# Kernel optimization log

Measured on AMD Instinct MI355X. Metric: run time of the kernel, lower is better.

## Reference

```python
import jax, jax.numpy as jnp
import numpy as np

T, H = 4096, 2048

def _glorot(key, shape):
    return jax.random.uniform(key, shape, minval=-1.0, maxval=1.0) * jnp.sqrt(2.0 / sum(shape))

def setup_inputs() -> dict:
    key = jax.random.key(0)
    k_x, k_a, k_b = jax.random.split(key, 3)
    x_seq = jax.random.normal(k_x, (T, H), dtype=jnp.float32)
    a_diag = _glorot(k_a, (H,)).astype(jnp.float32)        # (H,)
    b_mat = _glorot(k_b, (H, H)).astype(jnp.float32)       # (H, H)
    return {"x_seq": x_seq, "a_diag": a_diag, "b_mat": b_mat}

def _power_kernel(a_diag, length):
    # kernel[h, k] = a_diag[h] ** k for k in [0, length).
    # Computed via cumprod (identical math to jnp.power with integer exponents,
    # but well-defined for negative a_diag and differentiable).
    h = a_diag.shape[0]
    ones = jnp.ones((h, 1), dtype=a_diag.dtype)
    pows = jnp.cumprod(jnp.broadcast_to(a_diag[:, None], (h, length - 1)), axis=1)
    return jnp.concatenate([ones, pows], axis=1)[:, None, :]  # (H, 1, T)

def reference(x_seq, a_diag, b_mat):
    seq_len, hidden_size = x_seq.shape
    s = b_mat.T @ x_seq.T                                  # (H, T)
    s_padded = jnp.pad(s, ((0, 0), (seq_len - 1, 0)))[None, :, :]  # (1, H, 2T-1)
    kernel = _power_kernel(a_diag, seq_len)                # (H, 1, T)
    kernel_flipped = jnp.flip(kernel, axis=-1)
    conv_out = jax.lax.conv_general_dilated(
        s_padded, kernel_flipped,
        window_strides=(1,), padding="VALID",
        dimension_numbers=("NCT", "OIT", "NCT"),
        feature_group_count=hidden_size,
    )                                                      # (1, H, T)
    return conv_out[0].T                                   # (T, H)
```

## Files before the change

### kernel.cpp

```cpp
#include <hip/hip_runtime.h>
#include <cstdint>
#include <cstddef>

typedef short bf16x8 __attribute__((ext_vector_type(8)));
typedef float f32x4 __attribute__((ext_vector_type(4)));

__device__ __forceinline__ unsigned short f2bf(float f) {
    union { float f; uint32_t u; } v; v.f = f;
    uint32_t r = v.u + 0x7FFFu + ((v.u >> 16) & 1u);
    return (unsigned short)(r >> 16);
}

__device__ __forceinline__ float bf2f(unsigned short u) {
    union { uint32_t u; float f; } v; v.u = (uint32_t)u << 16;
    return v.f;
}


__global__ void prep_kernel(const float* __restrict__ X,
                            unsigned short* __restrict__ Xbf, int n4,
                            const float* __restrict__ B,
                            unsigned short* __restrict__ Bt, int H,
                            int castBlocks) {
    if ((int)blockIdx.x < castBlocks) {
        int i = blockIdx.x * 256 + threadIdx.x;
        if (i < n4) {
            float4 v = ((const float4*)X)[i];
            ushort4 o;
            o.x = f2bf(v.x); o.y = f2bf(v.y); o.z = f2bf(v.z); o.w = f2bf(v.w);
            ((ushort4*)Xbf)[i] = o;
        }
        return;
    }
    __shared__ float tile[32][33];
    int tb = blockIdx.x - castBlocks;
    int tilesPerRow = H / 32;
    int bx = (tb % tilesPerRow) * 32;
    int by = (tb / tilesPerRow) * 32;
    int tx = threadIdx.x & 31, ty = threadIdx.x >> 5;
#pragma unroll
    for (int i = 0; i < 32; i += 8)
        tile[ty + i][tx] = B[(size_t)(by + ty + i) * H + bx + tx];
    __syncthreads();
#pragma unroll
    for (int i = 0; i < 32; i += 8)
        Bt[(size_t)(bx + ty + i) * H + by + tx] = f2bf(tile[tx][ty + i]);
}


__global__ __launch_bounds__(256, 2) void gemm_sk_bf16out(
    const unsigned short* __restrict__ A,
    const unsigned short* __restrict__ Bt,
    unsigned short* __restrict__ S0, unsigned short* __restrict__ S1,
    int M, int N, int K, int gridM, int gridN)
{
    __shared__ __attribute__((aligned(16))) unsigned short sA[256 * 64];
    __shared__ __attribute__((aligned(16))) unsigned short sB[128 * 64];

    const int tid  = threadIdx.x;
    const int wave = tid >> 6;
    const int lane = tid & 63;

    int b = blockIdx.x;
    int mt, nt, kt;
    if ((gridM & 7) == 0) {
        int x = b & 7, g = b >> 3;
        int mPerX = gridM >> 3;
        int ml = g % mPerX, g2 = g / mPerX;
        nt = g2 % gridN;
        kt = g2 / gridN;
        mt = x * mPerX + ml;
    } else {
        mt = b % gridM;
        nt = (b / gridM) % gridN;
        kt = b / (gridM * gridN);
    }
    const int m0 = mt * 256;
    const int n0 = nt * 128;
    const int ksize = K / 2;
    const int kbase = kt * ksize;

    const int srow = lane >> 3;
    const int scol = ((lane & 7) ^ srow) * 8;

    const int quad = lane >> 4;
    const int l16  = lane & 15;
    const int wm = wave >> 1;
    const int wn = wave & 1;
    const int s7 = l16 & 7;
    const int c0 = (quad ^ s7) * 16;
    const int c1 = ((quad + 4) ^ s7) * 16;

    f32x4 acc[8][4];
#pragma unroll
    for (int i = 0; i < 8; ++i)
#pragma unroll
        for (int j = 0; j < 4; ++j)
            acc[i][j] = (f32x4){0.f, 0.f, 0.f, 0.f};

    const unsigned short* Ab = A  + (size_t)m0 * K;
    const unsigned short* Bb = Bt + (size_t)n0 * K;

    const int rA = (wm * 16 + (l16 >> 3)) * 1024 + s7 * 128;
    const int rB = (wn * 8  + (l16 >> 3)) * 1024 + s7 * 128;

    for (int k0 = kbase; k0 < kbase + ksize; k0 += 64) {
#pragma unroll
        for (int i = 0; i < 8; ++i) {
            const int t = wave * 8 + i;
            const unsigned short* ga = Ab + (size_t)(t * 8 + srow) * K + (k0 + scol);
            __builtin_amdgcn_global_load_lds(
                (const __attribute__((address_space(1))) void*)ga,
                (__attribute__((address_space(3))) void*)(sA + t * 512),
                16, 0, 0);
        }
#pragma unroll
        for (int i = 0; i < 4; ++i) {
            const int t = wave * 4 + i;
            const unsigned short* gb = Bb + (size_t)(t * 8 + srow) * K + (k0 + scol);
            __builtin_amdgcn_global_load_lds(
                (const __attribute__((address_space(1))) void*)gb,
                (__attribute__((address_space(3))) void*)(sB + t * 512),
                16, 0, 0);
        }
        __syncthreads();

#pragma unroll
        for (int kk = 0; kk < 2; ++kk) {
            const int co = kk ? c1 : c0;
            bf16x8 af[8], bfr[4];
#pragma unroll
            for (int im = 0; im < 8; ++im)
                af[im] = *(const bf16x8*)((const char*)sA + rA + im * 2048 + co);
#pragma unroll
            for (int in = 0; in < 4; ++in)
                bfr[in] = *(const bf16x8*)((const char*)sB + rB + in * 2048 + co);
#pragma unroll
            for (int im = 0; im < 8; ++im)
#pragma unroll
                for (int in = 0; in < 4; ++in)
                    acc[im][in] = __builtin_amdgcn_mfma_f32_16x16x32_bf16(
                        af[im], bfr[in], acc[im][in], 0, 0, 0);
        }
        __syncthreads();
    }

    unsigned short* __restrict__ S = (kt == 0) ? S0 : S1;
#pragma unroll
    for (int im = 0; im < 8; ++im) {
#pragma unroll
        for (int in = 0; in < 4; ++in) {
            int col = n0 + wn * 64 + in * 16 + l16;
#pragma unroll
            for (int r = 0; r < 4; ++r) {
                int row = m0 + wm * 128 + im * 16 + quad * 4 + r;
                S[(size_t)row * N + col] = f2bf(acc[im][in][r]);
            }
        }
    }
}


__device__ __forceinline__ void stage_tile128(
    const unsigned short* __restrict__ Ab, const unsigned short* __restrict__ Bb,
    unsigned short* sAp, unsigned short* sBp,
    int wave, int srow, int scol, int k0, int K)
{
#pragma unroll
    for (int i = 0; i < 4; ++i) {
        const int t = wave * 4 + i;
        const unsigned short* ga = Ab + (size_t)(t * 8 + srow) * K + (k0 + scol);
        __builtin_amdgcn_global_load_lds(
            (const __attribute__((address_space(1))) void*)ga,
            (__attribute__((address_space(3))) void*)(sAp + t * 512),
            16, 0, 0);
        const unsigned short* gb = Bb + (size_t)(t * 8 + srow) * K + (k0 + scol);
        __builtin_amdgcn_global_load_lds(
            (const __attribute__((address_space(1))) void*)gb,
            (__attribute__((address_space(3))) void*)(sBp + t * 512),
            16, 0, 0);
    }
}

__global__ __launch_bounds__(256, 4) void gemm_f32out(
    const unsigned short* __restrict__ A,
    const unsigned short* __restrict__ Bt,
    float* __restrict__ C, int M, int N, int K, int gridM)
{
    __shared__ __attribute__((aligned(16))) unsigned short sA[128 * 64];
    __shared__ __attribute__((aligned(16))) unsigned short sB[128 * 64];

    const int tid  = threadIdx.x;
    const int wave = tid >> 6;
    const int lane = tid & 63;

    int b = blockIdx.x;
    int mt, nt;
    if ((gridM & 7) == 0) {
        int x = b & 7, g = b >> 3;
        int mPerX = gridM >> 3;
        mt = x * mPerX + (g % mPerX);
        nt = g / mPerX;
    } else {
        mt = b % gridM;
        nt = b / gridM;
    }
    const int m0 = mt * 128;
    const int n0 = nt * 128;

    const int srow = lane >> 3;
    const int scol = ((lane & 7) ^ srow) * 8;
    const int quad = lane >> 4;
    const int l16  = lane & 15;
    const int wm = wave >> 1;
    const int wn = wave & 1;
    const int s7 = l16 & 7;
    const int rbaseA = (wm * 8 + (l16 >> 3)) * 1024 + s7 * 128;
    const int rbaseB = (wn * 8 + (l16 >> 3)) * 1024 + s7 * 128;
    const int coff0 = (quad ^ s7) * 16;
    const int coff1 = ((quad + 4) ^ s7) * 16;

    f32x4 acc[4][4];
#pragma unroll
    for (int i = 0; i < 4; ++i)
#pragma unroll
        for (int j = 0; j < 4; ++j)
            acc[i][j] = (f32x4){0.f, 0.f, 0.f, 0.f};

    const unsigned short* Ab = A  + (size_t)m0 * K;
    const unsigned short* Bb = Bt + (size_t)n0 * K;

    for (int k0 = 0; k0 < K; k0 += 64) {
        stage_tile128(Ab, Bb, sA, sB, wave, srow, scol, k0, K);
        __syncthreads();
        bf16x8 af[2][4], bfr[2][4];
#pragma unroll
        for (int t = 0; t < 4; ++t) {
            const char* pa = (const char*)sA + rbaseA + t * 2048;
            af[0][t]  = *(const bf16x8*)(pa + coff0);
            af[1][t]  = *(const bf16x8*)(pa + coff1);
            const char* pb = (const char*)sB + rbaseB + t * 2048;
            bfr[0][t] = *(const bf16x8*)(pb + coff0);
            bfr[1][t] = *(const bf16x8*)(pb + coff1);
        }
#pragma unroll
        for (int kk = 0; kk < 2; ++kk)
#pragma unroll
            for (int im = 0; im < 4; ++im)
#pragma unroll
                for (int in = 0; in < 4; ++in)
                    acc[im][in] = __builtin_amdgcn_mfma_f32_16x16x32_bf16(
                        af[kk][im], bfr[kk][in], acc[im][in], 0, 0, 0);
        __syncthreads();
    }

#pragma unroll
    for (int im = 0; im < 4; ++im)
#pragma unroll
        for (int in = 0; in < 4; ++in) {
            int col = n0 + wn * 64 + in * 16 + l16;
#pragma unroll
            for (int r = 0; r < 4; ++r) {
                int row = m0 + wm * 64 + im * 16 + quad * 4 + r;
                C[(size_t)row * N + col] = acc[im][in][r];
            }
        }
}


__global__ void scan_splitk_bf16(const unsigned short* __restrict__ S0,
                                 const unsigned short* __restrict__ S1,
                                 const float* __restrict__ a_diag,
                                 float* __restrict__ out,
                                 int H2, int chunk) {
    int tid = blockIdx.x * blockDim.x + threadIdx.x;
    int hp = tid % H2, c = tid / H2;
    float2 av = ((const float2*)a_diag)[hp];
    const ushort2* S0v = (const ushort2*)S0;
    const ushort2* S1v = (const ushort2*)S1;
    float2* outv = (float2*)out;

    float y0 = 0.f, y1 = 0.f;
    if (c > 0) {
        size_t r0 = (size_t)c * chunk - 8;
#pragma unroll
        for (int i = 0; i < 8; ++i) {
            size_t idx = (r0 + i) * H2 + hp;
            ushort2 u = S0v[idx], w = S1v[idx];
            y0 = fmaf(av.x, y0, bf2f(u.x) + bf2f(w.x));
            y1 = fmaf(av.y, y1, bf2f(u.y) + bf2f(w.y));
        }
    }
    size_t idx = (size_t)c * chunk * H2 + hp;
    ushort2 u = S0v[idx], w = S1v[idx];
    for (int t = 0; t < chunk - 1; ++t) {
        size_t idx2 = idx + H2;
        ushort2 un = S0v[idx2], wn = S1v[idx2];
        y0 = fmaf(av.x, y0, bf2f(u.x) + bf2f(w.x));
        y1 = fmaf(av.y, y1, bf2f(u.y) + bf2f(w.y));
        outv[idx] = make_float2(y0, y1);
        u = un; w = wn; idx = idx2;
    }
    y0 = fmaf(av.x, y0, bf2f(u.x) + bf2f(w.x));
    y1 = fmaf(av.y, y1, bf2f(u.y) + bf2f(w.y));
    outv[idx] = make_float2(y0, y1);
}


__global__ void scan_init_kernel(const float* __restrict__ S,
                                 const float* __restrict__ a_diag,
                                 float* __restrict__ yinit,
                                 int H, int chunk, int W) {
    int tid = blockIdx.x * blockDim.x + threadIdx.x;
    int h = tid % H, c = tid / H;
    float a = a_diag[h];
    float y = 0.f;
    if (c > 0) {
        int t0 = c * chunk;
        for (int t = t0 - W; t < t0; ++t)
            y = fmaf(a, y, S[(size_t)t * H + h]);
    }
    yinit[(size_t)c * H + h] = y;
}

__global__ void scan_run_kernel(const float* __restrict__ yinit,
                                const float* __restrict__ a_diag,
                                float* __restrict__ out,
                                int H, int chunk) {
    int tid = blockIdx.x * blockDim.x + threadIdx.x;
    int h = tid % H, c = tid / H;
    float a = a_diag[h];
    float y = yinit[(size_t)c * H + h];
    size_t base = (size_t)c * chunk * H + h;
    float s = out[base];
#pragma unroll 4
    for (int t = 0; t < chunk - 1; ++t) {
        float snext = out[base + (size_t)(t + 1) * H];
        y = fmaf(a, y, s);
        out[base + (size_t)t * H] = y;
        s = snext;
    }
    y = fmaf(a, y, s);
    out[base + (size_t)(chunk - 1) * H] = y;
}


__global__ void gemm_fallback(const float* __restrict__ X, const float* __restrict__ B,
                              float* __restrict__ C, int M, int N, int K) {
    __shared__ float sA[16][17];
    __shared__ float sB[16][17];
    int tx = threadIdx.x, ty = threadIdx.y;
    int row = blockIdx.y * 16 + ty, col = blockIdx.x * 16 + tx;
    float acc = 0.f;
    for (int k0 = 0; k0 < K; k0 += 16) {
        sA[ty][tx] = (row < M && k0 + tx < K) ? X[(size_t)row * K + k0 + tx] : 0.f;
        sB[ty][tx] = (k0 + ty < K && col < N) ? B[(size_t)(k0 + ty) * N + col] : 0.f;
        __syncthreads();
#pragma unroll
        for (int kk = 0; kk < 16; ++kk) acc += sA[ty][kk] * sB[kk][tx];
        __syncthreads();
    }
    if (row < M && col < N) C[(size_t)row * N + col] = acc;
}

__global__ void scan_serial(float* __restrict__ out, const float* __restrict__ a_diag,
                            int T, int H) {
    int h = blockIdx.x * blockDim.x + threadIdx.x;
    if (h >= H) return;
    float a = a_diag[h], y = 0.f;
    for (int t = 0; t < T; ++t) {
        y = fmaf(a, y, out[(size_t)t * H + h]);
        out[(size_t)t * H + h] = y;
    }
}


extern "C" void kernel_launch(void* const* d_in, const int* in_sizes, int n_in,
                              void* d_out, int out_size, void* d_ws, size_t ws_size,
                              hipStream_t stream) {
    const float* x = (const float*)d_in[0];
    const float* a = (const float*)d_in[1];
    const float* b = (const float*)d_in[2];
    float* out = (float*)d_out;

    const int H = in_sizes[1];
    const int T = in_sizes[0] / H;
    const int M = T, N = H, K = H;

    const int CHUNK = 16, W = 12;

    size_t xbf_elems = (size_t)M * K;
    size_t bt_elems  = (size_t)N * K;
    size_t MN = (size_t)M * N;
    int nchunks = (T % CHUNK == 0) ? T / CHUNK : 0;

    size_t need_sk  = (xbf_elems + bt_elems + 2 * MN) * 2 + 256;
    size_t need_mid = xbf_elems * 2 + bt_elems * 2 + 256;

    bool shape_ok = (M % 128 == 0) && (N % 128 == 0) && (K % 128 == 0) &&
                    (H % 32 == 0) && nchunks > 0 && ((xbf_elems % 4) == 0) &&
                    (((size_t)nchunks * H) % 256 == 0);
    int gridMf = M / 128;
    int gridM  = (M % 256 == 0) ? M / 256 : 0;
    int gridN  = N / 128;

    int n4 = (int)(xbf_elems / 4);
    int castBlocks = (n4 + 255) / 256;
    int transBlocks = (H % 32 == 0) ? (H / 32) * (H / 32) : 0;

    int H2 = H / 2;
    size_t nth2 = (size_t)nchunks * H2;

    if (shape_ok && gridM > 0 && (gridM % 8 == 0) && (H % 4 == 0) &&
        (nth2 % 256 == 0) && ws_size >= need_sk) {
        unsigned short* Xbf = (unsigned short*)d_ws;
        unsigned short* Bt  = Xbf + xbf_elems;
        unsigned short* S0  = Bt + bt_elems;
        unsigned short* S1  = S0 + MN;

        prep_kernel<<<castBlocks + transBlocks, 256, 0, stream>>>(
            x, Xbf, n4, b, Bt, H, castBlocks);

        gemm_sk_bf16out<<<gridM * gridN * 2, 256, 0, stream>>>(
            Xbf, Bt, S0, S1, M, N, K, gridM, gridN);

        scan_splitk_bf16<<<(int)(nth2 / 256), 256, 0, stream>>>(
            S0, S1, a, out, H2, CHUNK);
    } else if (shape_ok && ws_size >= need_mid &&
               ((size_t)nchunks * H * 4 <= xbf_elems * 2)) {
        unsigned short* Xbf = (unsigned short*)d_ws;
        unsigned short* Bt  = Xbf + xbf_elems;
        float* yinit = (float*)d_ws;

        prep_kernel<<<castBlocks + transBlocks, 256, 0, stream>>>(
            x, Xbf, n4, b, Bt, H, castBlocks);

        gemm_f32out<<<gridMf * gridN, 256, 0, stream>>>(
            Xbf, Bt, out, M, N, K, gridMf);

        int nth = nchunks * H;
        scan_init_kernel<<<nth / 256, 256, 0, stream>>>(out, a, yinit, H, CHUNK, W);
        scan_run_kernel<<<nth / 256, 256, 0, stream>>>(yinit, a, out, H, CHUNK);
    } else {
        dim3 tb(16, 16), tg((N + 15) / 16, (M + 15) / 16);
        gemm_fallback<<<tg, tb, 0, stream>>>(x, b, out, M, N, K);
        scan_serial<<<(H + 255) / 256, 256, 0, stream>>>(out, a, T, H);
    }
}
```

Baseline: 139.8 us.

## Add 256x256 eight-phase pipelined split-K GEMM with direct global-to-LDS loads

Adds a new bf16 GEMM kernel that uses 512 threads and 256x256 output tiles. It stages operands with global_load_lds into 128KB of dynamic LDS using double buffering and an XOR swizzle, and interleaves LDS reads, async global loads and MFMA bursts across eight barrier-separated phases with setprio. The aim is to raise arithmetic intensity and hide global-memory latency better than the previous 256x128 split-K kernel. In exchange it needs high LDS and register use, which limits occupancy, and it issues many barriers.

```diff
diff --git a/kernel.cpp b/kernel.cpp
--- a/kernel.cpp
+++ b/kernel.cpp
@@ -45,6 +45,202 @@
 #pragma unroll
     for (int i = 0; i < 32; i += 8)
         Bt[(size_t)(bx + ty + i) * H + by + tx] = f2bf(tile[tx][ty + i]);
+}
+
+
+#define G8_FENCE __builtin_amdgcn_sched_barrier(0)
+#define G8_BAR   __builtin_amdgcn_s_barrier()
+#define G8_LGKM0 asm volatile("s_waitcnt lgkmcnt(0)" ::: "memory")
+#define G8_VM4   asm volatile("s_waitcnt vmcnt(4)" ::: "memory")
+#define G8_VM0   asm volatile("s_waitcnt vmcnt(0)" ::: "memory")
+
+#define G8_STAGE(gbase, lbase, h, k0) do {                                    \
+    const int c0_ = (h) * 16 + wave;                                          \
+    const int c1_ = c0_ + 8;                                                  \
+    __builtin_amdgcn_global_load_lds(                                         \
+        (const __attribute__((address_space(1))) void*)                       \
+            ((gbase) + (size_t)(c0_ * 8 + srow) * K + ((k0) + scol)),         \
+        (__attribute__((address_space(3))) void*)                             \
+            ((lbase) + c0_ * 1024 + lane * 16), 16, 0, 0);                    \
+    __builtin_amdgcn_global_load_lds(                                         \
+        (const __attribute__((address_space(1))) void*)                       \
+            ((gbase) + (size_t)(c1_ * 8 + srow) * K + ((k0) + scol)),         \
+        (__attribute__((address_space(3))) void*)                             \
+            ((lbase) + c1_ * 1024 + lane * 16), 16, 0, 0);                    \
+} while (0)
+
+#define G8_LOAD_AF(buf, imh) do {                                             \
+    const char* p_ = (const char*)(buf) + rA + (imh) * 8192;                  \
+    af[0][0] = *(const bf16x8*)(p_ + 0 * 2048 + koff0);                       \
+    af[0][1] = *(const bf16x8*)(p_ + 0 * 2048 + koff1);                       \
+    af[1][0] = *(const bf16x8*)(p_ + 1 * 2048 + koff0);                       \
+    af[1][1] = *(const bf16x8*)(p_ + 1 * 2048 + koff1);                       \
+    af[2][0] = *(const bf16x8*)(p_ + 2 * 2048 + koff0);                       \
+    af[2][1] = *(const bf16x8*)(p_ + 2 * 2048 + koff1);                       \
+    af[3][0] = *(const bf16x8*)(p_ + 3 * 2048 + koff0);                       \
+    af[3][1] = *(const bf16x8*)(p_ + 3 * 2048 + koff1);                       \
+} while (0)
+
+#define G8_LOAD_BF(buf, inh) do {                                             \
+    const char* p_ = (const char*)(buf) + rB + (inh) * 4096;                  \
+    bq[inh][0][0] = *(const bf16x8*)(p_ + 0 * 2048 + koff0);                  \
+    bq[inh][0][1] = *(const bf16x8*)(p_ + 0 * 2048 + koff1);                  \
+    bq[inh][1][0] = *(const bf16x8*)(p_ + 1 * 2048 + koff0);                  \
+    bq[inh][1][1] = *(const bf16x8*)(p_ + 1 * 2048 + koff1);                  \
+} while (0)
+
+#define G8_MFMA(imh, inh) do {                                                \
+    _Pragma("unroll")                                                         \
+    for (int j_ = 0; j_ < 4; ++j_) {                                          \
+        acc[(imh)*4+j_][(inh)*2+0] = __builtin_amdgcn_mfma_f32_16x16x32_bf16( \
+            af[j_][0], bq[inh][0][0], acc[(imh)*4+j_][(inh)*2+0], 0, 0, 0);   \
+        acc[(imh)*4+j_][(inh)*2+0] = __builtin_amdgcn_mfma_f32_16x16x32_bf16( \
+            af[j_][1], bq[inh][0][1], acc[(imh)*4+j_][(inh)*2+0], 0, 0, 0);   \
+        acc[(imh)*4+j_][(inh)*2+1] = __builtin_amdgcn_mfma_f32_16x16x32_bf16( \
+            af[j_][0], bq[inh][1][0], acc[(imh)*4+j_][(inh)*2+1], 0, 0, 0);   \
+        acc[(imh)*4+j_][(inh)*2+1] = __builtin_amdgcn_mfma_f32_16x16x32_bf16( \
+            af[j_][1], bq[inh][1][1], acc[(imh)*4+j_][(inh)*2+1], 0, 0, 0);   \
+    }                                                                         \
+} while (0)
+
+#define G8_TAIL(MF, VMW) do {                                                 \
+    G8_FENCE;                                                                 \
+    G8_BAR;                                                                   \
+    G8_LGKM0; G8_FENCE;                                                       \
+    __builtin_amdgcn_s_setprio(1);                                            \
+    MF;                                                                       \
+    __builtin_amdgcn_s_setprio(0);                                            \
+    G8_FENCE; VMW;                                                            \
+    G8_BAR;                                                                   \
+    asm volatile("" ::: "memory");                                            \
+    G8_FENCE;                                                                 \
+} while (0)
+
+__global__ __launch_bounds__(512, 2) void gemm_8ph_bf16out(
+    const unsigned short* __restrict__ A,
+    const unsigned short* __restrict__ Bt,
+    unsigned short* __restrict__ S0, unsigned short* __restrict__ S1,
+    int M, int N, int K, int gridM2, int gridN2)
+{
+    extern __shared__ char smem[];
+
+    const int tid  = threadIdx.x;
+    const int wave = tid >> 6;
+    const int lane = tid & 63;
+
+    int b = blockIdx.x;
+    int mt, nt, kt;
+    if ((gridM2 & 7) == 0) {
+        int x = b & 7, g = b >> 3;
+        int mPerX = gridM2 >> 3;
+        int ml = g % mPerX, g2 = g / mPerX;
+        nt = g2 % gridN2;
+        kt = g2 / gridN2;
+        mt = x * mPerX + ml;
+    } else {
+        mt = b % gridM2;
+        nt = (b / gridM2) % gridN2;
+        kt = b / (gridM2 * gridN2);
+    }
+    const int m0 = mt * 256;
+    const int n0 = nt * 256;
+    const int ksize = K >> 1;
+    const int kbase = kt * ksize;
+    const int NT = ksize >> 6;
+    const int NI = NT >> 1;
+
+    const int wm = wave >> 2;
+    const int wn = wave & 3;
+    const int srow = lane >> 3;
+    const int scol = ((lane & 7) ^ srow) * 8;
+    const int quad = lane >> 4;
+    const int l16  = lane & 15;
+    const int s7   = l16 & 7;
+    const int rA = (wm * 16 + (l16 >> 3)) * 1024 + s7 * 128;
+    const int rB = (wn * 8  + (l16 >> 3)) * 1024 + s7 * 128;
+    const int koff0 = (quad ^ s7) * 16;
+    const int koff1 = ((quad + 4) ^ s7) * 16;
+
+    char* const A0L = smem;
+    char* const A1L = smem + 32768;
+    char* const B0L = smem + 65536;
+    char* const B1L = smem + 98304;
+
+    const unsigned short* const Ag = A  + (size_t)m0 * K;
+    const unsigned short* const Bg = Bt + (size_t)n0 * K;
+
+    f32x4 acc[8][4];
+#pragma unroll
+    for (int i = 0; i < 8; ++i)
+#pragma unroll
+        for (int j = 0; j < 4; ++j)
+            acc[i][j] = (f32x4){0.f, 0.f, 0.f, 0.f};
+    bf16x8 af[4][2];
+    bf16x8 bq[2][2][2];
+
+    G8_STAGE(Bg, B0L, 0, kbase);
+    G8_STAGE(Bg, B0L, 1, kbase);
+    G8_STAGE(Ag, A0L, 0, kbase);
+    G8_STAGE(Ag, A0L, 1, kbase);
+    G8_STAGE(Bg, B1L, 0, kbase + 64);
+    G8_STAGE(Bg, B1L, 1, kbase + 64);
+    G8_FENCE; G8_VM4;
+    G8_BAR;
+    asm volatile("" ::: "memory");
+    G8_FENCE;
+
+#pragma unroll 1
+    for (int it = 0; it < NI; ++it) {
+        const int c0t = it * 2;
+        int t1 = c0t + 1; if (t1 > NT - 1) t1 = NT - 1;
+        int t2 = c0t + 2; if (t2 > NT - 1) t2 = NT - 1;
+        int t3 = c0t + 3; if (t3 > NT - 1) t3 = NT - 1;
+        const int k1 = kbase + t1 * 64;
+        const int k2 = kbase + t2 * 64;
+        const int k3 = kbase + t3 * 64;
+
+        G8_LOAD_AF(A0L, 0);
+        G8_LOAD_BF(B0L, 0);
+        G8_STAGE(Ag, A1L, 0, k1);
+        G8_TAIL(G8_MFMA(0, 0), (void)0);
+        G8_LOAD_BF(B0L, 1);
+        G8_STAGE(Ag, A1L, 1, k1);
+        G8_TAIL(G8_MFMA(0, 1), (void)0);
+        G8_LOAD_AF(A0L, 1);
+        G8_STAGE(Bg, B0L, 0, k2);
+        G8_TAIL(G8_MFMA(1, 1), (void)0);
+        G8_STAGE(Bg, B0L, 1, k2);
+        G8_TAIL(G8_MFMA(1, 0), G8_VM4);
+
+        G8_LOAD_AF(A1L, 0);
+        G8_LOAD_BF(B1L, 0);
+        G8_STAGE(Ag, A0L, 0, k2);
+        G8_TAIL(G8_MFMA(0, 0), (void)0);
+        G8_LOAD_BF(B1L, 1);
+        G8_STAGE(Ag, A0L, 1, k2);
+        G8_TAIL(G8_MFMA(0, 1), (void)0);
+        G8_LOAD_AF(A1L, 1);
+        G8_STAGE(Bg, B1L, 0, k3);
+        G8_TAIL(G8_MFMA(1, 1), (void)0);
+        G8_STAGE(Bg, B1L, 1, k3);
+        G8_TAIL(G8_MFMA(1, 0), G8_VM4);
+    }
+
+    G8_VM0;
+
+    unsigned short* __restrict__ S = (kt == 0) ? S0 : S1;
+#pragma unroll
+    for (int im = 0; im < 8; ++im) {
+#pragma unroll
+        for (int in = 0; in < 4; ++in) {
+            const int col = n0 + wn * 64 + in * 16 + l16;
+#pragma unroll
+            for (int r = 0; r < 4; ++r) {
+                const int row = m0 + wm * 128 + im * 16 + quad * 4 + r;
+                S[(size_t)row * N + col] = f2bf(acc[im][in][r]);
+            }
+        }
+    }
 }
 
 
@@ -403,6 +599,9 @@
     int gridMf = M / 128;
     int gridM  = (M % 256 == 0) ? M / 256 : 0;
     int gridN  = N / 128;
+    int gridM8 = (M % 256 == 0) ? M / 256 : 0;
+    int gridN8 = (N % 256 == 0) ? N / 256 : 0;
+    bool k8ok  = (K % 256 == 0) && (K >= 256);
 
     int n4 = (int)(xbf_elems / 4);
     int castBlocks = (n4 + 255) / 256;
@@ -411,8 +610,31 @@
     int H2 = H / 2;
     size_t nth2 = (size_t)nchunks * H2;
 
-    if (shape_ok && gridM > 0 && (gridM % 8 == 0) && (H % 4 == 0) &&
+    if (shape_ok && gridM8 > 0 && gridN8 > 0 && k8ok && (H % 4 == 0) &&
         (nth2 % 256 == 0) && ws_size >= need_sk) {
+        unsigned short* Xbf = (unsigned short*)d_ws;
+        unsigned short* Bt  = Xbf + xbf_elems;
+        unsigned short* S0  = Bt + bt_elems;
+        unsigned short* S1  = S0 + MN;
+
+        static bool g8attr = false;
+        if (!g8attr) {
+            (void)hipFuncSetAttribute((const void*)gemm_8ph_bf16out,
+                                      hipFuncAttributeMaxDynamicSharedMemorySize,
+                                      131072);
+            g8attr = true;
+        }
+
+        prep_kernel<<<castBlocks + transBlocks, 256, 0, stream>>>(
+            x, Xbf, n4, b, Bt, H, castBlocks);
+
+        gemm_8ph_bf16out<<<gridM8 * gridN8 * 2, 512, 131072, stream>>>(
+            Xbf, Bt, S0, S1, M, N, K, gridM8, gridN8);
+
+        scan_splitk_bf16<<<(int)(nth2 / 256), 256, 0, stream>>>(
+            S0, S1, a, out, H2, CHUNK);
+    } else if (shape_ok && gridM > 0 && (gridM % 8 == 0) && (H % 4 == 0) &&
+               (nth2 % 256 == 0) && ws_size >= need_sk) {
         unsigned short* Xbf = (unsigned short*)d_ws;
         unsigned short* Bt  = Xbf + xbf_elems;
         unsigned short* S0  = Bt + bt_elems;
```

Measured after the change: 139.9 us. Within noise of the previous version (+0.1%).
